# Optimization experiments

Hardware: AMD Instinct MI355X
Metric: run time of the kernel (lower is better)

The kernel has to match this reference:

```python
import jax, jax.numpy as jnp
import numpy as np

THETA = 10000.0
MASK_FILL = -60000.0

def _rope(x):
    # lucidrains rotary_embedding_torch semantics: interleaved pairs, full-dim rotation
    S, D = x.shape[-2], x.shape[-1]
    inv_freq = 1.0 / (THETA ** (jnp.arange(0, D, 2, dtype=jnp.float32) / D))  # [D/2]
    freqs = jnp.arange(S, dtype=jnp.float32)[:, None] * inv_freq[None, :]     # [S, D/2]
    freqs = jnp.repeat(freqs, 2, axis=-1)                                     # [S, D] (each freq twice)
    cos, sin = jnp.cos(freqs), jnp.sin(freqs)
    xr = x.reshape(x.shape[:-1] + (D // 2, 2))
    rot_half = jnp.stack((-xr[..., 1], xr[..., 0]), axis=-1).reshape(x.shape)  # (x1,x2)->(-x2,x1)
    return x * cos + rot_half * sin

def setup_inputs() -> dict:
    key = jax.random.key(0)
    kq, kk, kv, km = jax.random.split(key, 4)
    B, H, S, D = 4, 16, 2048, 128
    return {
        "query": jax.random.normal(kq, (B, H, S, D), dtype=jnp.float32),
        "key": jax.random.normal(kk, (B, H, S, D), dtype=jnp.float32),
        "value": jax.random.normal(kv, (B, H, S, D), dtype=jnp.float32),
        "mask": jax.random.randint(km, (1, 1, S, S), 0, 2, dtype=jnp.int32),
    }

def reference(query, key, value, mask):
    q = _rope(query)
    k = _rope(key)
    scale = 1.0 / jnp.sqrt(jnp.float32(q.shape[-1]))
    scores = jnp.einsum('bhqd,bhkd->bhqk', q, k) * scale
    scores = jnp.where(mask == 0, jnp.float32(MASK_FILL), scores)
    p_attn = jax.nn.softmax(scores, axis=-1)
    out = jnp.einsum('bhqk,bhkd->bhqd', p_attn, value)
    return out, p_attn
```

## Files before the change

kernel.cpp:

```cpp
#include <hip/hip_runtime.h>
#include <hip/hip_fp16.h>
#include <cstdint>
#include <cstddef>

#define Bn 4
#define Hn 16
#define Sn 2048
#define Dn 128
#define MSHIFT 8.0f

typedef _Float16 half8  __attribute__((ext_vector_type(8)));
typedef float    f32x16 __attribute__((ext_vector_type(16)));
typedef float    f32x4v __attribute__((ext_vector_type(4)));
typedef unsigned uint4v __attribute__((ext_vector_type(4)));

__device__ __forceinline__ int pk_f16(float a, float b){
  auto h = __builtin_amdgcn_cvt_pkrtz(a, b);
  return __builtin_bit_cast(int, h);
}


__global__ void k_prep0(float2* __restrict__ tab,
                        const int* __restrict__ mask, unsigned* __restrict__ mtb){
  const int bid = blockIdx.x;
  if (bid < 512){
    const int idx = bid*256 + threadIdx.x;
    const int i = idx & 63, s = idx >> 6;
    const double invf = exp(-(double)i * (9.210340371976184 / 64.0));
    const double ang  = (double)s * invf;
    float2 cs; cs.x = (float)cos(ang); cs.y = (float)sin(ang);
    tab[idx] = cs;
  } else {
    const int g = (bid - 512)*256 + threadIdx.x;
    const int k = g & (Sn-1), q32 = g >> 11;
    unsigned bits = 0u;
    for (int j = 0; j < 32; ++j)
      bits |= (mask[(size_t)(q32*32 + j)*Sn + k] != 0 ? 1u : 0u) << j;
    mtb[g] = bits;
  }
}


__global__ void k_pack(const float* __restrict__ q, const float* __restrict__ k,
                       const float2* __restrict__ tab,
                       half8* __restrict__ qp, half8* __restrict__ kp){
  const int t    = blockIdx.x*256 + threadIdx.x;
  const int lane = t & 63, ln = lane & 31, h = lane >> 5;
  const int dc   = (t >> 6) & 7;
  const int blk  = (t >> 9) & 63;
  const int bh   = t >> 15;
  const int s    = blk*32 + ln;
  const size_t roff = ((size_t)bh*Sn + s)*Dn + dc*16 + h*8;
  const float4 a0 = *(const float4*)(q + roff);
  const float4 a1 = *(const float4*)(q + roff + 4);
  const float4 b0 = *(const float4*)(k + roff);
  const float4 b1 = *(const float4*)(k + roff + 4);
  const float2* tb = tab + s*64 + dc*8 + h*4;
  const float2 c0 = tb[0], c1 = tb[1], c2 = tb[2], c3 = tb[3];
  const float SC = 0.08838834764831845f;
  half8 qo, ko;
  qo[0] = (_Float16)((a0.x*c0.x - a0.y*c0.y)*SC);
  qo[1] = (_Float16)((a0.y*c0.x + a0.x*c0.y)*SC);
  qo[2] = (_Float16)((a0.z*c1.x - a0.w*c1.y)*SC);
  qo[3] = (_Float16)((a0.w*c1.x + a0.z*c1.y)*SC);
  qo[4] = (_Float16)((a1.x*c2.x - a1.y*c2.y)*SC);
  qo[5] = (_Float16)((a1.y*c2.x + a1.x*c2.y)*SC);
  qo[6] = (_Float16)((a1.z*c3.x - a1.w*c3.y)*SC);
  qo[7] = (_Float16)((a1.w*c3.x + a1.z*c3.y)*SC);
  ko[0] = (_Float16)(b0.x*c0.x - b0.y*c0.y);
  ko[1] = (_Float16)(b0.y*c0.x + b0.x*c0.y);
  ko[2] = (_Float16)(b0.z*c1.x - b0.w*c1.y);
  ko[3] = (_Float16)(b0.w*c1.x + b0.z*c1.y);
  ko[4] = (_Float16)(b1.x*c2.x - b1.y*c2.y);
  ko[5] = (_Float16)(b1.y*c2.x + b1.x*c2.y);
  ko[6] = (_Float16)(b1.z*c3.x - b1.w*c3.y);
  ko[7] = (_Float16)(b1.w*c3.x + b1.z*c3.y);
  qp[t] = qo;
  kp[t] = ko;
}


__global__ __launch_bounds__(512, 2) void attn_psv(
    const half8* __restrict__ qp, const half8* __restrict__ kp,
    const unsigned* __restrict__ mtb, const float* __restrict__ v,
    half8* __restrict__ wfrag, float* __restrict__ rinvb,
    half8* __restrict__ vp)
{
  const int bid = blockIdx.x;
  const int tid = threadIdx.x;

  if (bid % 9 == 0){
    const int p_id = bid / 9;
    const int work = ((p_id & 7) << 6) + (p_id >> 3);
    const int bh   = work >> 3;
    const int qg   = work & 7;
    const int w    = tid >> 6;
    const int l    = tid & 63;
    const int ln   = l & 31;
    const int h    = l >> 5;
    const int qb   = qg*8 + w;
    const int strip = bh*64 + qb;

    half8 qf[8];
#pragma unroll
    for (int dc = 0; dc < 8; ++dc)
      qf[dc] = qp[(((size_t)bh*64 + qb)*8 + dc)*64 + l];

    const unsigned* mrow = mtb + (size_t)qb*Sn;
    half8* wbase = wfrag + (size_t)strip*128*64;
    float L = 0.f;

    for (int kt = 0; kt < 64; ++kt){
      const half8* kf = kp + (((size_t)bh*64 + kt)*8)*64 + l;
      f32x16 a;
#pragma unroll
      for (int i = 0; i < 16; ++i) a[i] = 0.f;
#pragma unroll
      for (int dc = 0; dc < 8; ++dc)
        a = __builtin_amdgcn_mfma_f32_32x32x16_f16(kf[(size_t)dc*64], qf[dc], a, 0, 0, 0);

#pragma unroll
      for (int mm = 0; mm < 4; ++mm){
        const uint4v dw = *(const uint4v*)(mrow + kt*32 + mm*8 + h*4);
#pragma unroll
        for (int aa = 0; aa < 4; ++aa){
          const int r = mm*4 + aa;
          const float s = ((dw[aa] >> ln) & 1u) ? a[r] : -1.0e30f;
          const float u = __expf(s - MSHIFT);
          a[r] = u;
          L += u;
        }
      }

      int pk2[4][2];
#pragma unroll
      for (int b = 0; b < 4; ++b){
        pk2[b][0] = pk_f16(a[4*b+0], a[4*b+1]);
        pk2[b][1] = pk_f16(a[4*b+2], a[4*b+3]);
      }

#pragma unroll
      for (int t16 = 0; t16 < 2; ++t16){
        const int P00 = pk2[2*t16+0][0];
        const int P01 = pk2[2*t16+0][1];
        const int P10 = pk2[2*t16+1][0];
        const int P11 = pk2[2*t16+1][1];
        const int S00 = __shfl_xor(P00, 32, 64);
        const int S01 = __shfl_xor(P01, 32, 64);
        const int S10 = __shfl_xor(P10, 32, 64);
        const int S11 = __shfl_xor(P11, 32, 64);
        int4 bi;
        bi.x = h ? S10 : P00;
        bi.y = h ? S11 : P01;
        bi.z = h ? P10 : S00;
        bi.w = h ? P11 : S01;
        wbase[(size_t)(kt*2 + t16)*64 + l] = __builtin_bit_cast(half8, bi);
      }
    }

    L += __shfl_xor(L, 32, 64);
    if (l < 32) rinvb[(size_t)strip*32 + ln] = 1.0f / L;
  } else {
    const int v_id = bid - bid/9 - 1;
    const int t    = v_id*512 + tid;
    const int lane = t & 63, ln = lane & 31, h = lane >> 5;
    const int dt   = (t >> 6) & 3;
    const int k16  = (t >> 8) & 127;
    const int bh   = t >> 15;
    const size_t base = ((size_t)bh*Sn + k16*16 + h*8)*Dn + dt*32 + ln;
    half8 o;
#pragma unroll
    for (int j = 0; j < 8; ++j) o[j] = (_Float16)v[base + (size_t)j*Dn];
    vp[t] = o;
  }
}


__global__ __launch_bounds__(512, 2) void attn_ox(
    const half8* __restrict__ vp, const half8* __restrict__ wfrag,
    const float* __restrict__ rinvb, float* __restrict__ out,
    float* __restrict__ pout)
{
  __shared__ _Float16 ps[32][1032];
  __shared__ float rv[32];

  const int bid = blockIdx.x;
  const int tid = threadIdx.x;
  const int l   = tid & 63;
  const int ln  = l & 31;
  const int h   = l >> 5;

  if (bid % 17 == 0){
    const int work = bid / 17;
    const int bh   = work >> 3;
    const int qg   = work & 7;
    const int w    = tid >> 6;
    const int qb   = qg*8 + w;
    const int strip = bh*64 + qb;
    float* pt = (float*)&ps[0][0];
    #define PT(W,Q,C) pt[(((W)*32 + (Q))*34) + (C)]

    f32x16 oacc[4];
#pragma unroll
    for (int dt = 0; dt < 4; ++dt)
#pragma unroll
      for (int i = 0; i < 16; ++i) oacc[dt][i] = 0.f;

    const half8* wbase = wfrag + (size_t)strip*128*64;
    const half8* vbase = vp + (size_t)bh*128*4*64;

#pragma unroll 4
    for (int ks = 0; ks < 128; ++ks){
      const half8 bf = wbase[(size_t)ks*64 + l];
      const half8* vf = vbase + (size_t)ks*4*64 + l;
#pragma unroll
      for (int dt = 0; dt < 4; ++dt)
        oacc[dt] = __builtin_amdgcn_mfma_f32_32x32x16_f16(vf[(size_t)dt*64], bf, oacc[dt], 0, 0, 0);
    }

    const float rinv = rinvb[(size_t)strip*32 + ln];
#pragma unroll
    for (int dt = 0; dt < 4; ++dt)
#pragma unroll
      for (int i = 0; i < 16; ++i) oacc[dt][i] *= rinv;

    const size_t obase = ((size_t)bh*Sn + qb*32)*Dn;
    const int rq = l >> 3;
    const int rc = (l & 7) * 4;
#pragma unroll
    for (int dt = 0; dt < 4; ++dt){
#pragma unroll
      for (int g = 0; g < 4; ++g){
        const int c = g*8 + h*4;
        float2 e0, e1;
        e0.x = oacc[dt][4*g+0]; e0.y = oacc[dt][4*g+1];
        e1.x = oacc[dt][4*g+2]; e1.y = oacc[dt][4*g+3];
        *(float2*)&PT(w, ln, c)   = e0;
        *(float2*)&PT(w, ln, c+2) = e1;
      }
#pragma unroll
      for (int i = 0; i < 4; ++i){
        const int qq = i*8 + rq;
        const float2 t0 = *(const float2*)&PT(w, qq, rc);
        const float2 t1 = *(const float2*)&PT(w, qq, rc+2);
        f32x4v o4; o4.x = t0.x; o4.y = t0.y; o4.z = t1.x; o4.w = t1.y;
        __builtin_nontemporal_store(o4, (f32x4v*)(out + obase + (size_t)qq*Dn + dt*32 + rc));
      }
    }
    #undef PT
  } else {
    const int e_id  = bid - bid/17 - 1;
    const int strip = e_id >> 1;
    const int hh    = e_id & 1;
    const int w8    = tid >> 6;

    if (tid < 32) rv[tid] = rinvb[(size_t)strip*32 + tid];

#pragma unroll
    for (int i = 0; i < 8; ++i){
      const int cc = w8*8 + i;
      const half8 v = wfrag[((size_t)strip*128 + hh*64 + cc)*64 + l];
      *(half8*)&ps[ln][cc*16 + h*8] = v;
    }
    __syncthreads();

    const int bh = strip >> 6, qb = strip & 63;
    float* dst0 = pout + ((size_t)bh*Sn + qb*32)*Sn + hh*1024;
#pragma unroll
    for (int it = 0; it < 8; ++it){
      const int id  = it*512 + tid;
      const int row = id >> 7;
      const int c   = (id & 127) * 8;
      const half8 hv = *(const half8*)&ps[row][c];
      const float r = rv[row];
      f32x4v v0, v1;
      v0.x = (float)hv[0]*r; v0.y = (float)hv[1]*r; v0.z = (float)hv[2]*r; v0.w = (float)hv[3]*r;
      v1.x = (float)hv[4]*r; v1.y = (float)hv[5]*r; v1.z = (float)hv[6]*r; v1.w = (float)hv[7]*r;
      float* dp = dst0 + (size_t)row*Sn + c;
      __builtin_nontemporal_store(v0, (f32x4v*)dp);
      __builtin_nontemporal_store(v1, (f32x4v*)(dp + 4));
    }
  }
}


extern "C" void kernel_launch(void* const* d_in, const int* in_sizes, int n_in,
                              void* d_out, int out_size, void* d_ws, size_t ws_size,
                              hipStream_t stream)
{
  const float* dq = (const float*)d_in[0];
  const float* dk = (const float*)d_in[1];
  const float* dv = (const float*)d_in[2];
  const int*   dm = (const int*)d_in[3];

  char* ws = (char*)d_ws;
  float2*   tab  = (float2*)ws;
  half8*    qp   = (half8*)(ws + (size_t)(1u<<20));
  half8*    kp   = (half8*)(ws + (size_t)(1u<<20) + ((size_t)32<<20));
  half8*    vp   = (half8*)(ws + (size_t)(1u<<20) + ((size_t)64<<20));
  unsigned* mtb  = (unsigned*)(ws + (size_t)(1u<<20) + ((size_t)96<<20));
  float*    rinvb= (float*)(ws + (size_t)(1u<<20) + ((size_t)97<<20));
  half8*    wfr  = (half8*)(ws + (size_t)(1u<<20) + ((size_t)98<<20));

  float* out  = (float*)d_out;
  float* pout = out + (size_t)Bn*Hn*Sn*Dn;

  k_prep0  <<<1024, 256, 0, stream>>>(tab, dm, mtb);
  k_pack   <<<8192, 256, 0, stream>>>(dq, dk, tab, qp, kp);
  attn_psv <<<4608, 512, 0, stream>>>(qp, kp, mtb, dv, wfr, rinvb, vp);
  attn_ox  <<<8704, 512, 0, stream>>>(vp, wfr, rinvb, out, pout);
}
```

Before: 845.7 us.

## Split attention into two batch-head halves and overlap PV/expand with score pass

Splits the work by batch-head into two halves across three kernels. The middle kernel runs the MFMA- and exp-heavy score pass and V packing for the second half alongside the bandwidth-heavy PV matmul and fp32 probability expansion for the first half. The aim is to overlap compute-bound and store-bound phases that previously ran in separate serialized kernels. The cost is an extra launch, larger mixed blocks that may hurt occupancy or scheduling, and one idle block slot in every 27.

```diff
diff --git a/kernel.cpp b/kernel.cpp
--- a/kernel.cpp
+++ b/kernel.cpp
@@ -80,103 +80,239 @@
 }
 
 
+__device__ __forceinline__ void ps_body(
+    int p_id, int sbh,
+    const half8* __restrict__ qp, const half8* __restrict__ kp,
+    const unsigned* __restrict__ mtb, half8* __restrict__ wfrag,
+    float* __restrict__ rinvb, int tid)
+{
+  const int work = ((p_id & 7) << 5) + (p_id >> 3);
+  const int bh   = sbh + (work >> 3);
+  const int qg   = work & 7;
+  const int w    = tid >> 6;
+  const int l    = tid & 63;
+  const int ln   = l & 31;
+  const int h    = l >> 5;
+  const int qb   = qg*8 + w;
+  const int strip = bh*64 + qb;
+
+  half8 qf[8];
+#pragma unroll
+  for (int dc = 0; dc < 8; ++dc)
+    qf[dc] = qp[(((size_t)bh*64 + qb)*8 + dc)*64 + l];
+
+  const unsigned* mrow = mtb + (size_t)qb*Sn;
+  half8* wbase = wfrag + (size_t)strip*128*64;
+  float L = 0.f;
+
+  for (int kt = 0; kt < 64; ++kt){
+    const half8* kf = kp + (((size_t)bh*64 + kt)*8)*64 + l;
+    f32x16 a;
+#pragma unroll
+    for (int i = 0; i < 16; ++i) a[i] = 0.f;
+#pragma unroll
+    for (int dc = 0; dc < 8; ++dc)
+      a = __builtin_amdgcn_mfma_f32_32x32x16_f16(kf[(size_t)dc*64], qf[dc], a, 0, 0, 0);
+
+#pragma unroll
+    for (int mm = 0; mm < 4; ++mm){
+      const uint4v dw = *(const uint4v*)(mrow + kt*32 + mm*8 + h*4);
+#pragma unroll
+      for (int aa = 0; aa < 4; ++aa){
+        const int r = mm*4 + aa;
+        const float s = ((dw[aa] >> ln) & 1u) ? a[r] : -1.0e30f;
+        const float u = __expf(s - MSHIFT);
+        a[r] = u;
+        L += u;
+      }
+    }
+
+    int pk2[4][2];
+#pragma unroll
+    for (int b = 0; b < 4; ++b){
+      pk2[b][0] = pk_f16(a[4*b+0], a[4*b+1]);
+      pk2[b][1] = pk_f16(a[4*b+2], a[4*b+3]);
+    }
+
+#pragma unroll
+    for (int t16 = 0; t16 < 2; ++t16){
+      const int P00 = pk2[2*t16+0][0];
+      const int P01 = pk2[2*t16+0][1];
+      const int P10 = pk2[2*t16+1][0];
+      const int P11 = pk2[2*t16+1][1];
+      const int S00 = __shfl_xor(P00, 32, 64);
+      const int S01 = __shfl_xor(P01, 32, 64);
+      const int S10 = __shfl_xor(P10, 32, 64);
+      const int S11 = __shfl_xor(P11, 32, 64);
+      int4 bi;
+      bi.x = h ? S10 : P00;
+      bi.y = h ? S11 : P01;
+      bi.z = h ? P10 : S00;
+      bi.w = h ? P11 : S01;
+      wbase[(size_t)(kt*2 + t16)*64 + l] = __builtin_bit_cast(half8, bi);
+    }
+  }
+
+  L += __shfl_xor(L, 32, 64);
+  if (l < 32) rinvb[(size_t)strip*32 + ln] = 1.0f / L;
+}
+
+__device__ __forceinline__ void vpack_body(
+    int v_id, const float* __restrict__ v, half8* __restrict__ vp, int tid)
+{
+  const int t    = v_id*512 + tid;
+  const int lane = t & 63, ln = lane & 31, h = lane >> 5;
+  const int dt   = (t >> 6) & 3;
+  const int k16  = (t >> 8) & 127;
+  const int bh   = t >> 15;
+  const size_t base = ((size_t)bh*Sn + k16*16 + h*8)*Dn + dt*32 + ln;
+  half8 o;
+#pragma unroll
+  for (int j = 0; j < 8; ++j) o[j] = (_Float16)v[base + (size_t)j*Dn];
+  vp[t] = o;
+}
+
+__device__ __forceinline__ void o_body(
+    int work, int sbh,
+    const half8* __restrict__ vp, const half8* __restrict__ wfrag,
+    const float* __restrict__ rinvb, float* __restrict__ out,
+    float* pt, int tid)
+{
+  const int bh   = sbh + (work >> 3);
+  const int qg   = work & 7;
+  const int w    = tid >> 6;
+  const int l    = tid & 63;
+  const int ln   = l & 31;
+  const int h    = l >> 5;
+  const int qb   = qg*8 + w;
+  const int strip = bh*64 + qb;
+  #define PT(W,Q,C) pt[(((W)*32 + (Q))*34) + (C)]
+
+  f32x16 oacc[4];
+#pragma unroll
+  for (int dt = 0; dt < 4; ++dt)
+#pragma unroll
+    for (int i = 0; i < 16; ++i) oacc[dt][i] = 0.f;
+
+  const half8* wbase = wfrag + (size_t)strip*128*64;
+  const half8* vbase = vp + (size_t)bh*128*4*64;
+
+#pragma unroll 4
+  for (int ks = 0; ks < 128; ++ks){
+    const half8 bf = wbase[(size_t)ks*64 + l];
+    const half8* vf = vbase + (size_t)ks*4*64 + l;
+#pragma unroll
+    for (int dt = 0; dt < 4; ++dt)
+      oacc[dt] = __builtin_amdgcn_mfma_f32_32x32x16_f16(vf[(size_t)dt*64], bf, oacc[dt], 0, 0, 0);
+  }
+
+  const float rinv = rinvb[(size_t)strip*32 + ln];
+#pragma unroll
+  for (int dt = 0; dt < 4; ++dt)
+#pragma unroll
+    for (int i = 0; i < 16; ++i) oacc[dt][i] *= rinv;
+
+  const size_t obase = ((size_t)bh*Sn + qb*32)*Dn;
+  const int rq = l >> 3;
+  const int rc = (l & 7) * 4;
+#pragma unroll
+  for (int dt = 0; dt < 4; ++dt){
+#pragma unroll
+    for (int g = 0; g < 4; ++g){
+      const int c = g*8 + h*4;
+      float2 e0, e1;
+      e0.x = oacc[dt][4*g+0]; e0.y = oacc[dt][4*g+1];
+      e1.x = oacc[dt][4*g+2]; e1.y = oacc[dt][4*g+3];
+      *(float2*)&PT(w, ln, c)   = e0;
+      *(float2*)&PT(w, ln, c+2) = e1;
+    }
+#pragma unroll
+    for (int i = 0; i < 4; ++i){
+      const int qq = i*8 + rq;
+      const float2 t0 = *(const float2*)&PT(w, qq, rc);
+      const float2 t1 = *(const float2*)&PT(w, qq, rc+2);
+      f32x4v o4; o4.x = t0.x; o4.y = t0.y; o4.z = t1.x; o4.w = t1.y;
+      __builtin_nontemporal_store(o4, (f32x4v*)(out + obase + (size_t)qq*Dn + dt*32 + rc));
+    }
+  }
+  #undef PT
+}
+
+__device__ __forceinline__ void expand_body(
+    int e_id, int sbh,
+    const half8* __restrict__ wfrag, const float* __restrict__ rinvb,
+    float* __restrict__ pout, _Float16 (*ps)[1032], float* rv, int tid)
+{
+  const int strip = sbh*64 + (e_id >> 1);
+  const int hh    = e_id & 1;
+  const int l     = tid & 63;
+  const int w8    = tid >> 6;
+  const int ln    = l & 31;
+  const int h     = l >> 5;
+
+  if (tid < 32) rv[tid] = rinvb[(size_t)strip*32 + tid];
+
+#pragma unroll
+  for (int i = 0; i < 8; ++i){
+    const int cc = w8*8 + i;
+    const half8 v = wfrag[((size_t)strip*128 + hh*64 + cc)*64 + l];
+    *(half8*)&ps[ln][cc*16 + h*8] = v;
+  }
+  __syncthreads();
+
+  const int bh = strip >> 6, qb = strip & 63;
+  float* dst0 = pout + ((size_t)bh*Sn + qb*32)*Sn + hh*1024;
+#pragma unroll
+  for (int it = 0; it < 8; ++it){
+    const int id  = it*512 + tid;
+    const int row = id >> 7;
+    const int c   = (id & 127) * 8;
+    const half8 hv = *(const half8*)&ps[row][c];
+    const float r = rv[row];
+    f32x4v v0, v1;
+    v0.x = (float)hv[0]*r; v0.y = (float)hv[1]*r; v0.z = (float)hv[2]*r; v0.w = (float)hv[3]*r;
+    v1.x = (float)hv[4]*r; v1.y = (float)hv[5]*r; v1.z = (float)hv[6]*r; v1.w = (float)hv[7]*r;
+    float* dp = dst0 + (size_t)row*Sn + c;
+    __builtin_nontemporal_store(v0, (f32x4v*)dp);
+    __builtin_nontemporal_store(v1, (f32x4v*)(dp + 4));
+  }
+}
+
+
 __global__ __launch_bounds__(512, 2) void attn_psv(
     const half8* __restrict__ qp, const half8* __restrict__ kp,
     const unsigned* __restrict__ mtb, const float* __restrict__ v,
     half8* __restrict__ wfrag, float* __restrict__ rinvb,
-    half8* __restrict__ vp)
+    half8* __restrict__ vp, int sbh, int vbase)
 {
   const int bid = blockIdx.x;
   const int tid = threadIdx.x;
-
-  if (bid % 9 == 0){
-    const int p_id = bid / 9;
-    const int work = ((p_id & 7) << 6) + (p_id >> 3);
-    const int bh   = work >> 3;
-    const int qg   = work & 7;
-    const int w    = tid >> 6;
-    const int l    = tid & 63;
-    const int ln   = l & 31;
-    const int h    = l >> 5;
-    const int qb   = qg*8 + w;
-    const int strip = bh*64 + qb;
-
-    half8 qf[8];
-#pragma unroll
-    for (int dc = 0; dc < 8; ++dc)
-      qf[dc] = qp[(((size_t)bh*64 + qb)*8 + dc)*64 + l];
-
-    const unsigned* mrow = mtb + (size_t)qb*Sn;
-    half8* wbase = wfrag + (size_t)strip*128*64;
-    float L = 0.f;
-
-    for (int kt = 0; kt < 64; ++kt){
-      const half8* kf = kp + (((size_t)bh*64 + kt)*8)*64 + l;
-      f32x16 a;
-#pragma unroll
-      for (int i = 0; i < 16; ++i) a[i] = 0.f;
-#pragma unroll
-      for (int dc = 0; dc < 8; ++dc)
-        a = __builtin_amdgcn_mfma_f32_32x32x16_f16(kf[(size_t)dc*64], qf[dc], a, 0, 0, 0);
-
-#pragma unroll
-      for (int mm = 0; mm < 4; ++mm){
-        const uint4v dw = *(const uint4v*)(mrow + kt*32 + mm*8 + h*4);
-#pragma unroll
-        for (int aa = 0; aa < 4; ++aa){
-          const int r = mm*4 + aa;
-          const float s = ((dw[aa] >> ln) & 1u) ? a[r] : -1.0e30f;
-          const float u = __expf(s - MSHIFT);
-          a[r] = u;
-          L += u;
-        }
-      }
-
-      int pk2[4][2];
-#pragma unroll
-      for (int b = 0; b < 4; ++b){
-        pk2[b][0] = pk_f16(a[4*b+0], a[4*b+1]);
-        pk2[b][1] = pk_f16(a[4*b+2], a[4*b+3]);
-      }
-
-#pragma unroll
-      for (int t16 = 0; t16 < 2; ++t16){
-        const int P00 = pk2[2*t16+0][0];
-        const int P01 = pk2[2*t16+0][1];
-        const int P10 = pk2[2*t16+1][0];
-        const int P11 = pk2[2*t16+1][1];
-        const int S00 = __shfl_xor(P00, 32, 64);
-        const int S01 = __shfl_xor(P01, 32, 64);
-        const int S10 = __shfl_xor(P10, 32, 64);
-        const int S11 = __shfl_xor(P11, 32, 64);
-        int4 bi;
-        bi.x = h ? S10 : P00;
-        bi.y = h ? S11 : P01;
-        bi.z = h ? P10 : S00;
-        bi.w = h ? P11 : S01;
-        wbase[(size_t)(kt*2 + t16)*64 + l] = __builtin_bit_cast(half8, bi);
-      }
-    }
-
-    L += __shfl_xor(L, 32, 64);
-    if (l < 32) rinvb[(size_t)strip*32 + ln] = 1.0f / L;
-  } else {
-    const int v_id = bid - bid/9 - 1;
-    const int t    = v_id*512 + tid;
-    const int lane = t & 63, ln = lane & 31, h = lane >> 5;
-    const int dt   = (t >> 6) & 3;
-    const int k16  = (t >> 8) & 127;
-    const int bh   = t >> 15;
-    const size_t base = ((size_t)bh*Sn + k16*16 + h*8)*Dn + dt*32 + ln;
-    half8 o;
-#pragma unroll
-    for (int j = 0; j < 8; ++j) o[j] = (_Float16)v[base + (size_t)j*Dn];
-    vp[t] = o;
-  }
-}
-
-
-__global__ __launch_bounds__(512, 2) void attn_ox(
+  const int g = bid / 9, r = bid % 9;
+  if (r == 0) ps_body(g, sbh, qp, kp, mtb, wfrag, rinvb, tid);
+  else        vpack_body(vbase + g*8 + (r-1), v, vp, tid);
+}
+
+
+__global__ __launch_bounds__(512, 2) void attn_mix(
+    const half8* __restrict__ qp, const half8* __restrict__ kp,
+    const unsigned* __restrict__ mtb, const float* __restrict__ v,
+    half8* __restrict__ wfrag, float* __restrict__ rinvb,
+    half8* __restrict__ vp, float* __restrict__ out, float* __restrict__ pout)
+{
+  __shared__ _Float16 ps[32][1032];
+  __shared__ float rv[32];
+
+  const int bid = blockIdx.x;
+  const int tid = threadIdx.x;
+  const int g = bid / 27, r = bid % 27;
+  if (r == 0)       ps_body(g, 32, qp, kp, mtb, wfrag, rinvb, tid);
+  else if (r <= 8)  vpack_body(2048 + g*8 + (r-1), v, vp, tid);
+  else if (r == 9)  o_body(g, 0, vp, wfrag, rinvb, out, (float*)&ps[0][0], tid);
+  else if (r <= 25) expand_body(g*16 + (r-10), 0, wfrag, rinvb, pout, ps, rv, tid);
+}
+
+
+__global__ __launch_bounds__(512, 2) void attn_ox2(
     const half8* __restrict__ vp, const half8* __restrict__ wfrag,
     const float* __restrict__ rinvb, float* __restrict__ out,
     float* __restrict__ pout)
@@ -186,101 +322,8 @@
 
   const int bid = blockIdx.x;
   const int tid = threadIdx.x;
-  const int l   = tid & 63;
-  const int ln  = l & 31;
-  const int h   = l >> 5;
-
-  if (bid % 17 == 0){
-    const int work = bid / 17;
-    const int bh   = work >> 3;
-    const int qg   = work & 7;
-    const int w    = tid >> 6;
-    const int qb   = qg*8 + w;
-    const int strip = bh*64 + qb;
-    float* pt = (float*)&ps[0][0];
-    #define PT(W,Q,C) pt[(((W)*32 + (Q))*34) + (C)]
-
-    f32x16 oacc[4];
-#pragma unroll
-    for (int dt = 0; dt < 4; ++dt)
-#pragma unroll
-      for (int i = 0; i < 16; ++i) oacc[dt][i] = 0.f;
-
-    const half8* wbase = wfrag + (size_t)strip*128*64;
-    const half8* vbase = vp + (size_t)bh*128*4*64;
-
-#pragma unroll 4
-    for (int ks = 0; ks < 128; ++ks){
-      const half8 bf = wbase[(size_t)ks*64 + l];
-      const half8* vf = vbase + (size_t)ks*4*64 + l;
-#pragma unroll
-      for (int dt = 0; dt < 4; ++dt)
-        oacc[dt] = __builtin_amdgcn_mfma_f32_32x32x16_f16(vf[(size_t)dt*64], bf, oacc[dt], 0, 0, 0);
-    }
-
-    const float rinv = rinvb[(size_t)strip*32 + ln];
-#pragma unroll
-    for (int dt = 0; dt < 4; ++dt)
-#pragma unroll
-      for (int i = 0; i < 16; ++i) oacc[dt][i] *= rinv;
-
-    const size_t obase = ((size_t)bh*Sn + qb*32)*Dn;
-    const int rq = l >> 3;
-    const int rc = (l & 7) * 4;
-#pragma unroll
-    for (int dt = 0; dt < 4; ++dt){
-#pragma unroll
-      for (int g = 0; g < 4; ++g){
-        const int c = g*8 + h*4;
-        float2 e0, e1;
-        e0.x = oacc[dt][4*g+0]; e0.y = oacc[dt][4*g+1];
-        e1.x = oacc[dt][4*g+2]; e1.y = oacc[dt][4*g+3];
-        *(float2*)&PT(w, ln, c)   = e0;
-        *(float2*)&PT(w, ln, c+2) = e1;
-      }
-#pragma unroll
-      for (int i = 0; i < 4; ++i){
-        const int qq = i*8 + rq;
-        const float2 t0 = *(const float2*)&PT(w, qq, rc);
-        const float2 t1 = *(const float2*)&PT(w, qq, rc+2);
-        f32x4v o4; o4.x = t0.x; o4.y = t0.y; o4.z = t1.x; o4.w = t1.y;
-        __builtin_nontemporal_store(o4, (f32x4v*)(out + obase + (size_t)qq*Dn + dt*32 + rc));
-      }
-    }
-    #undef PT
-  } else {
-    const int e_id  = bid - bid/17 - 1;
-    const int strip = e_id >> 1;
-    const int hh    = e_id & 1;
-    const int w8    = tid >> 6;
-
-    if (tid < 32) rv[tid] = rinvb[(size_t)strip*32 + tid];
-
-#pragma unroll
-    for (int i = 0; i < 8; ++i){
-      const int cc = w8*8 + i;
-      const half8 v = wfrag[((size_t)strip*128 + hh*64 + cc)*64 + l];
-      *(half8*)&ps[ln][cc*16 + h*8] = v;
-    }
-    __syncthreads();
-
-    const int bh = strip >> 6, qb = strip & 63;
-    float* dst0 = pout + ((size_t)bh*Sn + qb*32)*Sn + hh*1024;
-#pragma unroll
-    for (int it = 0; it < 8; ++it){
-      const int id  = it*512 + tid;
-      const int row = id >> 7;
-      const int c   = (id & 127) * 8;
-      const half8 hv = *(const half8*)&ps[row][c];
-      const float r = rv[row];
-      f32x4v v0, v1;
-      v0.x = (float)hv[0]*r; v0.y = (float)hv[1]*r; v0.z = (float)hv[2]*r; v0.w = (float)hv[3]*r;
-      v1.x = (float)hv[4]*r; v1.y = (float)hv[5]*r; v1.z = (float)hv[6]*r; v1.w = (float)hv[7]*r;
-      float* dp = dst0 + (size_t)row*Sn + c;
-      __builtin_nontemporal_store(v0, (f32x4v*)dp);
-      __builtin_nontemporal_store(v1, (f32x4v*)(dp + 4));
-    }
-  }
+  if (bid % 17 == 0) o_body(bid/17, 32, vp, wfrag, rinvb, out, (float*)&ps[0][0], tid);
+  else               expand_body(bid - bid/17 - 1, 32, wfrag, rinvb, pout, ps, rv, tid);
 }
 
 
@@ -307,6 +350,7 @@
 
   k_prep0  <<<1024, 256, 0, stream>>>(tab, dm, mtb);
   k_pack   <<<8192, 256, 0, stream>>>(dq, dk, tab, qp, kp);
-  attn_psv <<<4608, 512, 0, stream>>>(qp, kp, mtb, dv, wfr, rinvb, vp);
-  attn_ox  <<<8704, 512, 0, stream>>>(vp, wfr, rinvb, out, pout);
-}
+  attn_psv <<<2304, 512, 0, stream>>>(qp, kp, mtb, dv, wfr, rinvb, vp, 0, 0);
+  attn_mix <<<6912, 512, 0, stream>>>(qp, kp, mtb, dv, wfr, rinvb, vp, out, pout);
+  attn_ox2 <<<4352, 512, 0, stream>>>(vp, wfr, rinvb, out, pout);
+}
```

Result: slower. 956.2 us (+13.1%).
